# Performance work log

Hardware: AMD Instinct MI355X
Metric: run time of the kernel (lower is better)

Reference implementation:

```python
import jax, jax.numpy as jnp
import numpy as np

N_NODES = 100000


def gcn_conv(x, W, b, edge_index, n_nodes):
    """PyG GCNConv: add self-loops, symmetric deg^-1/2 normalization,
    linear transform, scatter-sum aggregation, bias."""
    x = x @ W  # [N, out]
    src, dst = edge_index[0], edge_index[1]
    self_idx = jnp.arange(n_nodes, dtype=src.dtype)
    src = jnp.concatenate([src, self_idx])
    dst = jnp.concatenate([dst, self_idx])
    # in-degree (including self-loop) per destination node
    deg = jax.ops.segment_sum(jnp.ones_like(src, dtype=x.dtype), dst,
                              num_segments=n_nodes)
    dinv = jnp.where(deg > 0, jax.lax.rsqrt(deg), 0.0)
    norm = dinv[src] * dinv[dst]  # [E+N]
    msg = x[src] * norm[:, None]  # gather + scale, [E+N, out]
    out = jax.ops.segment_sum(msg, dst, num_segments=n_nodes)
    return out + b


def setup_inputs() -> dict:
    key = jax.random.key(0)
    ks = jax.random.split(key, 7)
    in_c, hid_c, out_c = 256, 128, 64
    n_edges, n_lbl = 1600000, 200000
    x = jax.random.normal(ks[0], (N_NODES, in_c), dtype=jnp.float32)
    edge_index = jax.random.randint(ks[1], (2, n_edges), 0, N_NODES, dtype=jnp.int64)
    edge_label_index = jax.random.randint(ks[2], (2, n_lbl), 0, N_NODES, dtype=jnp.int64)
    # Glorot-style init for GCN linear weights
    W1 = jax.random.normal(ks[3], (in_c, hid_c), dtype=jnp.float32) / np.sqrt(in_c)
    b1 = jnp.zeros((hid_c,), dtype=jnp.float32)
    W2 = jax.random.normal(ks[4], (hid_c, out_c), dtype=jnp.float32) / np.sqrt(hid_c)
    b2 = jnp.zeros((out_c,), dtype=jnp.float32)
    return {"x": x, "edge_index": edge_index,
            "edge_label_index": edge_label_index,
            "W1": W1, "b1": b1, "W2": W2, "b2": b2}


def reference(x, edge_index, edge_label_index, W1, b1, W2, b2):
    n = x.shape[0]
    h = jax.nn.relu(gcn_conv(x, W1, b1, edge_index, n))
    z = gcn_conv(h, W2, b2, edge_index, n)  # [N, out_c]
    src, dst = edge_label_index[0], edge_label_index[1]
    return jnp.sum(z[src] * z[dst], axis=-1)  # [E_lbl]
```

## Files before the change

kernel.cpp:

```cpp
#include <hip/hip_runtime.h>
#include <hip/hip_bf16.h>

#define N_NODES 100000
#define N_EDGES 1600000
#define N_LBL   200000
#define C_IN    256
#define C_HID   128
#define C_OUT   64
#define SCAN_BLOCKS 391
#define NBUCKET 391
#define FILLA_EPB 2048

using u16 = unsigned short;
using u32 = unsigned int;
using u64 = unsigned long long;
using s64 = long long;

typedef __attribute__((ext_vector_type(8))) short bf16x8;
typedef __attribute__((ext_vector_type(4))) float f32x4;

__device__ __forceinline__ float bf2f(u16 h) {
    u32 u = ((u32)h) << 16;
    float f;
    __builtin_memcpy(&f, &u, 4);
    return f;
}
__device__ __forceinline__ u16 f2bf(float f) {
    u32 u;
    __builtin_memcpy(&u, &f, 4);
    u32 r = (u + 0x7fffu + ((u >> 16) & 1u)) >> 16;
    return (u16)r;
}
__device__ __forceinline__ void unpack_bf2(u32 p, float& lo, float& hi) {
    u32 l = p << 16;
    u32 h = p & 0xffff0000u;
    __builtin_memcpy(&lo, &l, 4);
    __builtin_memcpy(&hi, &h, 4);
}
__device__ __forceinline__ void acc4(u64 p, float& a0, float& a1,
                                     float& a2, float& a3) {
    u32 lo = (u32)p, hi = (u32)(p >> 32);
    float f0, f1, f2, f3;
    unpack_bf2(lo, f0, f1);
    unpack_bf2(hi, f2, f3);
    a0 += f0; a1 += f1; a2 += f2; a3 += f3;
}
__device__ __forceinline__ int geti(const void* p, s64 i, int i64) {
    return i64 ? (int)((const s64*)p)[i] : ((const int*)p)[i];
}
__device__ __forceinline__ int clampn(int v) {
    return ((u32)v < (u32)N_NODES) ? v : 0;
}

__device__ __forceinline__ void split8(const float4& a, const float4& b,
                                       bf16x8& hi8, bf16x8& lo8) {
    float va[8] = {a.x, a.y, a.z, a.w, b.x, b.y, b.z, b.w};
    u32 uh[4], ul[4];
#pragma unroll
    for (int p = 0; p < 4; ++p) {
        float x0 = va[2 * p], x1 = va[2 * p + 1];
        u32 u0, u1;
        __builtin_memcpy(&u0, &x0, 4);
        __builtin_memcpy(&u1, &x1, 4);
        u32 h0 = u0 & 0xffff0000u, h1 = u1 & 0xffff0000u;
        float f0, f1;
        __builtin_memcpy(&f0, &h0, 4);
        __builtin_memcpy(&f1, &h1, 4);
        float l0 = x0 - f0, l1 = x1 - f1;
        u32 w0, w1;
        __builtin_memcpy(&w0, &l0, 4);
        __builtin_memcpy(&w1, &l1, 4);
        uh[p] = (u0 >> 16) | h1;
        ul[p] = (w0 >> 16) | (w1 & 0xffff0000u);
    }
    struct U { u32 w[4]; };
    U H = {{uh[0], uh[1], uh[2], uh[3]}};
    U L = {{ul[0], ul[1], ul[2], ul[3]}};
    __builtin_memcpy(&hi8, &H, 16);
    __builtin_memcpy(&lo8, &L, 16);
}

__global__ void k_detect(const void* __restrict__ x, const void* __restrict__ ei,
                         int* __restrict__ flags) {
    const int lane = threadIdx.x & 63;
    const u16* xh = (const u16*)x;
    int cnt = 0;
#pragma unroll
    for (int k = 0; k < 4; ++k) {
        int i = 2 * (lane + 64 * k);
        u32 e = (xh[i] >> 7) & 0xFF;
        cnt += __builtin_popcountll(__ballot(e > 137));
    }
    const u32* ew = (const u32*)ei;
    int nz = __builtin_popcountll(__ballot(ew[2 * lane + 1] != 0));
    if (lane == 0) {
        flags[0] = (cnt > 16) ? 1 : 0;
        flags[1] = (nz == 0) ? 1 : 0;
    }
}

__global__ __launch_bounds__(256) void k_bcount(const void* __restrict__ ei,
                                                const int* __restrict__ flags,
                                                int* __restrict__ bcnt) {
    __shared__ int hist[NBUCKET];
    const int t = threadIdx.x;
    if (t < NBUCKET) hist[t] = 0;
    if (t + 256 < NBUCKET) hist[t + 256] = 0;
    __syncthreads();
    const s64 base = (s64)blockIdx.x * FILLA_EPB;
    const int i64 = flags[1];
#pragma unroll
    for (int j = 0; j < 8; ++j) {
        s64 e = base + t + 256 * j;
        if (e < N_EDGES) {
            int d = clampn(geti(ei, (s64)N_EDGES + e, i64));
            atomicAdd(&hist[d >> 8], 1);
        }
    }
    __syncthreads();
    if (t < NBUCKET && hist[t]) atomicAdd(&bcnt[t], hist[t]);
    if (t + 256 < NBUCKET && hist[t + 256]) atomicAdd(&bcnt[t + 256], hist[t + 256]);
}

__global__ __launch_bounds__(512) void k_bscan(const int* __restrict__ bcnt,
                                               int* __restrict__ bstart,
                                               int* __restrict__ gcur) {
    __shared__ int arr[512];
    const int t = threadIdx.x;
    int v = (t < NBUCKET) ? bcnt[t] : 0;
    arr[t] = v;
    __syncthreads();
#pragma unroll
    for (int off = 1; off < 512; off <<= 1) {
        int u = (t >= off) ? arr[t - off] : 0;
        __syncthreads();
        arr[t] += u;
        __syncthreads();
    }
    if (t < NBUCKET) {
        int ex = arr[t] - v;
        bstart[t] = ex;
        gcur[t]   = ex;
    }
    if (t == 511) bstart[NBUCKET] = arr[511];
}

__global__ __launch_bounds__(256) void k_fillA(const void* __restrict__ ei,
                                               const int* __restrict__ flags,
                                               int* __restrict__ gcur,
                                               u64* __restrict__ temp) {
    __shared__ int hist[NBUCKET];
    __shared__ int gbase[NBUCKET];
    const int t = threadIdx.x;
    if (t < NBUCKET) hist[t] = 0;
    if (t + 256 < NBUCKET) hist[t + 256] = 0;
    __syncthreads();
    const s64 base = (s64)blockIdx.x * FILLA_EPB;
    const int i64 = flags[1];
    int sv[8], dv[8], bk[8], off[8];
    bool val[8];
#pragma unroll
    for (int j = 0; j < 8; ++j) {
        s64 e = base + t + 256 * j;
        val[j] = (e < N_EDGES);
        if (val[j]) {
            sv[j] = clampn(geti(ei, e, i64));
            dv[j] = clampn(geti(ei, (s64)N_EDGES + e, i64));
            bk[j] = dv[j] >> 8;
            off[j] = atomicAdd(&hist[bk[j]], 1);
        }
    }
    __syncthreads();
    if (t < NBUCKET && hist[t]) gbase[t] = atomicAdd(&gcur[t], hist[t]);
    if (t + 256 < NBUCKET && hist[t + 256]) gbase[t + 256] = atomicAdd(&gcur[t + 256], hist[t + 256]);
    __syncthreads();
#pragma unroll
    for (int j = 0; j < 8; ++j) {
        if (val[j])
            temp[(size_t)(gbase[bk[j]] + off[j])] = ((u64)(u32)dv[j] << 32) | (u32)sv[j];
    }
}

__global__ __launch_bounds__(256) void k_deg2(const u64* __restrict__ temp,
                                              const int* __restrict__ bstart,
                                              int* __restrict__ deg) {
    __shared__ int dcnt[256];
    const int t = threadIdx.x;
    const int b = blockIdx.x;
    dcnt[t] = 0;
    __syncthreads();
    const int beg = bstart[b], end = bstart[b + 1];
    for (int e = beg + t; e < end; e += 256) {
        u32 d = (u32)(temp[e] >> 32);
        atomicAdd(&dcnt[d & 255], 1);
    }
    __syncthreads();
    int node = (b << 8) + t;
    if (node < N_NODES) deg[node] = dcnt[t];
}

__global__ __launch_bounds__(256) void k_fillB(const u64* __restrict__ temp,
                                               const int* __restrict__ bstart,
                                               const int* __restrict__ row_ptr,
                                               int* __restrict__ csr_src) {
    __shared__ int cur[256];
    const int t = threadIdx.x;
    const int b = blockIdx.x;
    int node = (b << 8) + t;
    cur[t] = (node < N_NODES) ? row_ptr[node] : 0;
    __syncthreads();
    const int beg = bstart[b], end = bstart[b + 1];
    for (int e = beg + t; e < end; e += 256) {
        u64 p = temp[e];
        u32 s = (u32)p, d = (u32)(p >> 32);
        int pos = atomicAdd(&cur[d & 255], 1);
        csr_src[pos] = (int)s;
    }
}

__global__ __launch_bounds__(256) void k_scan1(const int* __restrict__ deg,
                                               int* __restrict__ bsum) {
    __shared__ int red[256];
    const int t = threadIdx.x;
    int i = blockIdx.x * 256 + t;
    red[t] = (i < N_NODES) ? deg[i] : 0;
    __syncthreads();
#pragma unroll
    for (int off = 128; off > 0; off >>= 1) {
        if (t < off) red[t] += red[t + off];
        __syncthreads();
    }
    if (t == 0) bsum[blockIdx.x] = red[0];
}

__global__ __launch_bounds__(512) void k_scan2(const int* __restrict__ bsum,
                                               int* __restrict__ boff,
                                               int* __restrict__ row_ptr) {
    __shared__ int arr[512];
    const int t = threadIdx.x;
    int v = (t < SCAN_BLOCKS) ? bsum[t] : 0;
    arr[t] = v;
    __syncthreads();
#pragma unroll
    for (int off = 1; off < 512; off <<= 1) {
        int u = (t >= off) ? arr[t - off] : 0;
        __syncthreads();
        arr[t] += u;
        __syncthreads();
    }
    if (t < SCAN_BLOCKS) boff[t] = arr[t] - v;
    if (t == 511) row_ptr[N_NODES] = arr[511];
}

__global__ __launch_bounds__(256) void k_scan3(const int* __restrict__ deg,
                                               const int* __restrict__ boff,
                                               int* __restrict__ row_ptr,
                                               float* __restrict__ dinv) {
    __shared__ int arr[256];
    const int t = threadIdx.x;
    int i = blockIdx.x * 256 + t;
    int v = (i < N_NODES) ? deg[i] : 0;
    arr[t] = v;
    __syncthreads();
#pragma unroll
    for (int off = 1; off < 256; off <<= 1) {
        int u = (t >= off) ? arr[t - off] : 0;
        __syncthreads();
        arr[t] += u;
        __syncthreads();
    }
    if (i < N_NODES) {
        int run = boff[blockIdx.x] + arr[t] - v;
        row_ptr[i] = run;
        dinv[i]    = rsqrtf((float)v + 1.0f);
    }
}

__global__ __launch_bounds__(256) void k_w1t(const void* __restrict__ W1_,
                                             const int* __restrict__ flags,
                                             u16* __restrict__ w1t_hi,
                                             u16* __restrict__ w1t_lo) {
    int idx = blockIdx.x * 256 + threadIdx.x;
    int k = idx >> 7, n = idx & 127;
    float v = flags[0] ? ((const float*)W1_)[idx] : bf2f(((const u16*)W1_)[idx]);
    u32 uv;
    __builtin_memcpy(&uv, &v, 4);
    u32 hf = uv & 0xffff0000u;
    float hb;
    __builtin_memcpy(&hb, &hf, 4);
    float lo = v - hb;
    u32 ulo;
    __builtin_memcpy(&ulo, &lo, 4);
    w1t_hi[n * C_IN + k] = (u16)(uv >> 16);
    w1t_lo[n * C_IN + k] = (u16)(ulo >> 16);
}

__global__ __launch_bounds__(256) void k_w2t(const void* __restrict__ W2_,
                                             const int* __restrict__ flags,
                                             u16* __restrict__ w2t_hi,
                                             u16* __restrict__ w2t_lo) {
    int idx = blockIdx.x * 256 + threadIdx.x;
    int k = idx >> 6, n = idx & 63;
    float v = flags[0] ? ((const float*)W2_)[idx] : bf2f(((const u16*)W2_)[idx]);
    u32 uv;
    __builtin_memcpy(&uv, &v, 4);
    u32 hf = uv & 0xffff0000u;
    float hb;
    __builtin_memcpy(&hb, &hf, 4);
    float lo = v - hb;
    u32 ulo;
    __builtin_memcpy(&ulo, &lo, 4);
    w2t_hi[n * C_HID + k] = (u16)(uv >> 16);
    w2t_lo[n * C_HID + k] = (u16)(ulo >> 16);
}

__global__ __launch_bounds__(512) void k_gemm1_mfma(const void* __restrict__ xv_,
                                                    const u16* __restrict__ w1t_hi,
                                                    const u16* __restrict__ w1t_lo,
                                                    const float* __restrict__ dinv,
                                                    const int* __restrict__ flags,
                                                    u16* __restrict__ g0) {
    __shared__ u16 lds_hi[64 * 256];
    __shared__ u16 lds_lo[64 * 256];
    const int isf32 = flags[0];
    const int lane = threadIdx.x & 63;
    const int wid  = threadIdx.x >> 6;
    const int r0   = blockIdx.x * 256 + wid * 32;
    const int nbase = blockIdx.y * 64;

    {
        const u16* sh = w1t_hi + (size_t)nbase * C_IN;
        const u16* sl = w1t_lo + (size_t)nbase * C_IN;
        for (int g = threadIdx.x; g < 2048; g += 512) {
            int row = g >> 5;
            int off = (g & 31) << 4;
            int dst = row * 512 + (off ^ ((row & 7) << 4));
            *(uint4*)((char*)lds_hi + dst) =
                *(const uint4*)((const char*)(sh + (size_t)row * C_IN) + off);
            *(uint4*)((char*)lds_lo + dst) =
                *(const uint4*)((const char*)(sl + (size_t)row * C_IN) + off);
        }
    }
    __syncthreads();

    const int rowA = r0 + (lane & 15);
    const int rowB = rowA + 16;
    const int rlA  = (rowA < N_NODES) ? rowA : (N_NODES - 1);
    const int rlB  = (rowB < N_NODES) ? rowB : (N_NODES - 1);
    const int kh   = (lane >> 4) * 8;
    const int khb  = (lane >> 4) * 16;

    int rbase[4], rswz[4];
#pragma unroll
    for (int n = 0; n < 4; ++n) {
        int rloc = n * 16 + (lane & 15);
        rbase[n] = rloc * 512;
        rswz[n]  = (rloc & 7) << 4;
    }

    f32x4 acc[2][4];
#pragma unroll
    for (int g = 0; g < 2; ++g)
#pragma unroll
        for (int n = 0; n < 4; ++n) acc[g][n] = (f32x4){0.f, 0.f, 0.f, 0.f};

    if (isf32) {
        const float* apA = (const float*)xv_ + (size_t)rlA * C_IN + kh;
        const float* apB = (const float*)xv_ + (size_t)rlB * C_IN + kh;
        float4 xa0 = ((const float4*)apA)[0];
        float4 xa1 = ((const float4*)(apA + 4))[0];
        float4 xb0 = ((const float4*)apB)[0];
        float4 xb1 = ((const float4*)(apB + 4))[0];
#pragma unroll
        for (int k0 = 0; k0 < C_IN; k0 += 32) {
            bf16x8 bh[4], bl[4];
#pragma unroll
            for (int n = 0; n < 4; ++n) {
                int a = rbase[n] + ((k0 * 2 + khb) ^ rswz[n]);
                bh[n] = *(const bf16x8*)((const char*)lds_hi + a);
                bl[n] = *(const bf16x8*)((const char*)lds_lo + a);
            }
            float4 na0, na1, nb0, nb1;
            if (k0 + 32 < C_IN) {
                na0 = ((const float4*)(apA + k0 + 32))[0];
                na1 = ((const float4*)(apA + k0 + 36))[0];
                nb0 = ((const float4*)(apB + k0 + 32))[0];
                nb1 = ((const float4*)(apB + k0 + 36))[0];
            }
            bf16x8 ahiA, aloA, ahiB, aloB;
            split8(xa0, xa1, ahiA, aloA);
            split8(xb0, xb1, ahiB, aloB);
#pragma unroll
            for (int n = 0; n < 4; ++n) {
                acc[0][n] = __builtin_amdgcn_mfma_f32_16x16x32_bf16(ahiA, bl[n], acc[0][n], 0, 0, 0);
                acc[0][n] = __builtin_amdgcn_mfma_f32_16x16x32_bf16(aloA, bh[n], acc[0][n], 0, 0, 0);
                acc[0][n] = __builtin_amdgcn_mfma_f32_16x16x32_bf16(ahiA, bh[n], acc[0][n], 0, 0, 0);
                acc[1][n] = __builtin_amdgcn_mfma_f32_16x16x32_bf16(ahiB, bl[n], acc[1][n], 0, 0, 0);
                acc[1][n] = __builtin_amdgcn_mfma_f32_16x16x32_bf16(aloB, bh[n], acc[1][n], 0, 0, 0);
                acc[1][n] = __builtin_amdgcn_mfma_f32_16x16x32_bf16(ahiB, bh[n], acc[1][n], 0, 0, 0);
            }
            if (k0 + 32 < C_IN) { xa0 = na0; xa1 = na1; xb0 = nb0; xb1 = nb1; }
        }
    } else {
        const u16* apA = (const u16*)xv_ + (size_t)rlA * C_IN + kh;
        const u16* apB = (const u16*)xv_ + (size_t)rlB * C_IN + kh;
        bf16x8 aA = *(const bf16x8*)apA;
        bf16x8 aB = *(const bf16x8*)apB;
#pragma unroll
        for (int k0 = 0; k0 < C_IN; k0 += 32) {
            bf16x8 bh[4];
#pragma unroll
            for (int n = 0; n < 4; ++n) {
                int a = rbase[n] + ((k0 * 2 + khb) ^ rswz[n]);
                bh[n] = *(const bf16x8*)((const char*)lds_hi + a);
            }
            bf16x8 nA, nB;
            if (k0 + 32 < C_IN) {
                nA = *(const bf16x8*)(apA + k0 + 32);
                nB = *(const bf16x8*)(apB + k0 + 32);
            }
#pragma unroll
            for (int n = 0; n < 4; ++n) {
                acc[0][n] = __builtin_amdgcn_mfma_f32_16x16x32_bf16(aA, bh[n], acc[0][n], 0, 0, 0);
                acc[1][n] = __builtin_amdgcn_mfma_f32_16x16x32_bf16(aB, bh[n], acc[1][n], 0, 0, 0);
            }
            if (k0 + 32 < C_IN) { aA = nA; aB = nB; }
        }
    }

    const int ccol = lane & 15;
#pragma unroll
    for (int g = 0; g < 2; ++g) {
        const int crow0 = r0 + g * 16 + (lane >> 4) * 4;
#pragma unroll
        for (int i = 0; i < 4; ++i) {
            int r = crow0 + i;
            if (r < N_NODES) {
                float dv = dinv[r];
#pragma unroll
                for (int n = 0; n < 4; ++n)
                    g0[(size_t)r * C_HID + nbase + n * 16 + ccol] = f2bf(dv * acc[g][n][i]);
            }
        }
    }
}

__global__ __launch_bounds__(512) void k_gemm2_mfma(const float* __restrict__ h,
                                                    const u16* __restrict__ w2t_hi,
                                                    const u16* __restrict__ w2t_lo,
                                                    const float* __restrict__ dinv,
                                                    u16* __restrict__ g1) {
    __shared__ u16 lds_hi[64 * 128];
    __shared__ u16 lds_lo[64 * 128];
    const int lane = threadIdx.x & 63;
    const int wid  = threadIdx.x >> 6;
    const int r0   = blockIdx.x * 256 + wid * 32;

    {
        for (int g = threadIdx.x; g < 1024; g += 512) {
            int row = g >> 4;
            int off = (g & 15) << 4;
            int dst = row * 256 + (off ^ ((row & 7) << 4));
            *(uint4*)((char*)lds_hi + dst) =
                *(const uint4*)((const char*)(w2t_hi + (size_t)row * C_HID) + off);
            *(uint4*)((char*)lds_lo + dst) =
                *(const uint4*)((const char*)(w2t_lo + (size_t)row * C_HID) + off);
        }
    }
    __syncthreads();

    const int rowA = r0 + (lane & 15);
    const int rowB = rowA + 16;
    const int rlA  = (rowA < N_NODES) ? rowA : (N_NODES - 1);
    const int rlB  = (rowB < N_NODES) ? rowB : (N_NODES - 1);
    const int kh   = (lane >> 4) * 8;
    const int khb  = (lane >> 4) * 16;

    int rbase[4], rswz[4];
#pragma unroll
    for (int n = 0; n < 4; ++n) {
        int rloc = n * 16 + (lane & 15);
        rbase[n] = rloc * 256;
        rswz[n]  = (rloc & 7) << 4;
    }

    f32x4 acc[2][4];
#pragma unroll
    for (int g = 0; g < 2; ++g)
#pragma unroll
        for (int n = 0; n < 4; ++n) acc[g][n] = (f32x4){0.f, 0.f, 0.f, 0.f};

    const float* apA = h + (size_t)rlA * C_HID + kh;
    const float* apB = h + (size_t)rlB * C_HID + kh;

    float4 xa0 = ((const float4*)apA)[0];
    float4 xa1 = ((const float4*)(apA + 4))[0];
    float4 xb0 = ((const float4*)apB)[0];
    float4 xb1 = ((const float4*)(apB + 4))[0];
#pragma unroll
    for (int k0 = 0; k0 < C_HID; k0 += 32) {
        bf16x8 bh[4], bl[4];
#pragma unroll
        for (int n = 0; n < 4; ++n) {
            int a = rbase[n] + ((k0 * 2 + khb) ^ rswz[n]);
            bh[n] = *(const bf16x8*)((const char*)lds_hi + a);
            bl[n] = *(const bf16x8*)((const char*)lds_lo + a);
        }
        float4 na0, na1, nb0, nb1;
        if (k0 + 32 < C_HID) {
            na0 = ((const float4*)(apA + k0 + 32))[0];
            na1 = ((const float4*)(apA + k0 + 36))[0];
            nb0 = ((const float4*)(apB + k0 + 32))[0];
            nb1 = ((const float4*)(apB + k0 + 36))[0];
        }
        bf16x8 ahiA, aloA, ahiB, aloB;
        split8(xa0, xa1, ahiA, aloA);
        split8(xb0, xb1, ahiB, aloB);
#pragma unroll
        for (int n = 0; n < 4; ++n) {
            acc[0][n] = __builtin_amdgcn_mfma_f32_16x16x32_bf16(ahiA, bl[n], acc[0][n], 0, 0, 0);
            acc[0][n] = __builtin_amdgcn_mfma_f32_16x16x32_bf16(aloA, bh[n], acc[0][n], 0, 0, 0);
            acc[0][n] = __builtin_amdgcn_mfma_f32_16x16x32_bf16(ahiA, bh[n], acc[0][n], 0, 0, 0);
            acc[1][n] = __builtin_amdgcn_mfma_f32_16x16x32_bf16(ahiB, bl[n], acc[1][n], 0, 0, 0);
            acc[1][n] = __builtin_amdgcn_mfma_f32_16x16x32_bf16(aloB, bh[n], acc[1][n], 0, 0, 0);
            acc[1][n] = __builtin_amdgcn_mfma_f32_16x16x32_bf16(ahiB, bh[n], acc[1][n], 0, 0, 0);
        }
        if (k0 + 32 < C_HID) { xa0 = na0; xa1 = na1; xb0 = nb0; xb1 = nb1; }
    }

    const int ccol = lane & 15;
#pragma unroll
    for (int g = 0; g < 2; ++g) {
        const int crow0 = r0 + g * 16 + (lane >> 4) * 4;
#pragma unroll
        for (int i = 0; i < 4; ++i) {
            int r = crow0 + i;
            if (r < N_NODES) {
                float dv = dinv[r];
#pragma unroll
                for (int n = 0; n < 4; ++n)
                    g1[(size_t)r * C_OUT + n * 16 + ccol] = f2bf(dv * acc[g][n][i]);
            }
        }
    }
}

__global__ __launch_bounds__(256) void k_gather128(const int* __restrict__ row_ptr,
                                                   const int* __restrict__ csr_src,
                                                   const u64* __restrict__ g,
                                                   const void* __restrict__ bias_,
                                                   const float* __restrict__ dinv,
                                                   const int* __restrict__ flags,
                                                   float* __restrict__ out) {
    const int lane = threadIdx.x & 63;
    const int wid  = threadIdx.x >> 6;
    const int half = lane >> 5;
    const int jj   = lane & 31;
    const int node = blockIdx.x * 8 + wid * 2 + half;
    const u64* gp = g + jj;
    const int beg = row_ptr[node], end = row_ptr[node + 1];
    float a0 = 0.f, a1 = 0.f, a2 = 0.f, a3 = 0.f;
    int e = beg;
    for (; e + 4 <= end; e += 4) {
        int s0 = csr_src[e], s1 = csr_src[e + 1];
        int s2 = csr_src[e + 2], s3 = csr_src[e + 3];
        u64 p0 = gp[(size_t)s0 * 32];
        u64 p1 = gp[(size_t)s1 * 32];
        u64 p2 = gp[(size_t)s2 * 32];
        u64 p3 = gp[(size_t)s3 * 32];
        acc4(p0, a0, a1, a2, a3);
        acc4(p1, a0, a1, a2, a3);
        acc4(p2, a0, a1, a2, a3);
        acc4(p3, a0, a1, a2, a3);
    }
    for (; e < end; ++e) acc4(gp[(size_t)csr_src[e] * 32], a0, a1, a2, a3);
    acc4(gp[(size_t)node * 32], a0, a1, a2, a3);
    float b0, b1, b2, b3;
    if (flags[0]) {
        float4 bb = ((const float4*)bias_)[jj];
        b0 = bb.x; b1 = bb.y; b2 = bb.z; b3 = bb.w;
    } else {
        u64 bw = ((const u64*)bias_)[jj];
        unpack_bf2((u32)bw, b0, b1);
        unpack_bf2((u32)(bw >> 32), b2, b3);
    }
    float dv = dinv[node];
    float4 r;
    r.x = fmaxf(dv * a0 + b0, 0.f);
    r.y = fmaxf(dv * a1 + b1, 0.f);
    r.z = fmaxf(dv * a2 + b2, 0.f);
    r.w = fmaxf(dv * a3 + b3, 0.f);
    ((float4*)(out + (size_t)node * C_HID))[jj] = r;
}

__global__ __launch_bounds__(256) void k_gather64(const int* __restrict__ row_ptr,
                                                  const int* __restrict__ csr_src,
                                                  const u64* __restrict__ g,
                                                  const void* __restrict__ bias_,
                                                  const float* __restrict__ dinv,
                                                  const int* __restrict__ flags,
                                                  float* __restrict__ out) {
    const int lane = threadIdx.x & 63;
    const int wid  = threadIdx.x >> 6;
    const int q    = lane >> 4;
    const int jj   = lane & 15;
    const int node = blockIdx.x * 16 + wid * 4 + q;
    const u64* gp = g + jj;
    const int beg = row_ptr[node], end = row_ptr[node + 1];
    float a0 = 0.f, a1 = 0.f, a2 = 0.f, a3 = 0.f;
    int e = beg;
    for (; e + 4 <= end; e += 4) {
        int s0 = csr_src[e], s1 = csr_src[e + 1];
        int s2 = csr_src[e + 2], s3 = csr_src[e + 3];
        u64 p0 = gp[(size_t)s0 * 16];
        u64 p1 = gp[(size_t)s1 * 16];
        u64 p2 = gp[(size_t)s2 * 16];
        u64 p3 = gp[(size_t)s3 * 16];
        acc4(p0, a0, a1, a2, a3);
        acc4(p1, a0, a1, a2, a3);
        acc4(p2, a0, a1, a2, a3);
        acc4(p3, a0, a1, a2, a3);
    }
    for (; e < end; ++e) acc4(gp[(size_t)csr_src[e] * 16], a0, a1, a2, a3);
    acc4(gp[(size_t)node * 16], a0, a1, a2, a3);
    float b0, b1, b2, b3;
    if (flags[0]) {
        float4 bb = ((const float4*)bias_)[jj];
        b0 = bb.x; b1 = bb.y; b2 = bb.z; b3 = bb.w;
    } else {
        u64 bw = ((const u64*)bias_)[jj];
        unpack_bf2((u32)bw, b0, b1);
        unpack_bf2((u32)(bw >> 32), b2, b3);
    }
    float dv = dinv[node];
    float4 r;
    r.x = dv * a0 + b0;
    r.y = dv * a1 + b1;
    r.z = dv * a2 + b2;
    r.w = dv * a3 + b3;
    ((float4*)(out + (size_t)node * C_OUT))[jj] = r;
}

__global__ __launch_bounds__(256) void k_edgedot(const void* __restrict__ eli,
                                                 const int* __restrict__ flags,
                                                 const float* __restrict__ z,
                                                 void* __restrict__ out) {
    const int g16 = threadIdx.x >> 4;
    const int l16 = threadIdx.x & 15;
    const int e = blockIdx.x * 16 + g16;
    if (e >= N_LBL) return;
    const int i64 = flags[1];
    const int s = clampn(geti(eli, e, i64));
    const int d = clampn(geti(eli, (s64)N_LBL + e, i64));
    float4 zs = *(const float4*)(z + (size_t)s * C_OUT + l16 * 4);
    float4 zd = *(const float4*)(z + (size_t)d * C_OUT + l16 * 4);
    float v = zs.x * zd.x + zs.y * zd.y + zs.z * zd.z + zs.w * zd.w;
    v += __shfl_xor(v, 1, 64);
    v += __shfl_xor(v, 2, 64);
    v += __shfl_xor(v, 4, 64);
    v += __shfl_xor(v, 8, 64);
    if (l16 == 0) {
        if (flags[0]) ((float*)out)[e] = v;
        else          ((u16*)out)[e]   = f2bf(v);
    }
}

extern "C" void kernel_launch(void* const* d_in, const int* in_sizes, int n_in,
                              void* d_out, int out_size, void* d_ws, size_t ws_size,
                              hipStream_t stream) {
    const void* x   = d_in[0];
    const void* ei  = d_in[1];
    const void* eli = d_in[2];
    const void* W1  = d_in[3];
    const void* b1  = d_in[4];
    const void* W2  = d_in[5];
    const void* b2  = d_in[6];

    if (ws_size < 84800128) return;
    char* ws = (char*)d_ws;
    float* h       = (float*)ws;
    float* z       = (float*)ws;
    int*   bsum    = (int*)ws;
    int*   boff    = (int*)(ws + 4096);
    int*   bcnt    = (int*)(ws + 8192);
    int*   bstart  = (int*)(ws + 12288);
    int*   gcur    = (int*)(ws + 16384);
    u64*   temp    = (u64*)(ws + 1048576);
    u16*   g0      = (u16*)(ws + 51200000);
    u16*   g1      = (u16*)(ws + 51200000);
    float* dinv    = (float*)(ws + 76800000);
    int*   deg     = (int*)(ws + 77200000);
    u16*   w1t_hi  = (u16*)(ws + 77200000);
    u16*   w1t_lo  = (u16*)(ws + 77200000 + 65536);
    u16*   w2t_hi  = (u16*)(ws + 77200000 + 131072);
    u16*   w2t_lo  = (u16*)(ws + 77200000 + 147456);
    int*   row_ptr = (int*)(ws + 77600000);
    int*   csr_src = (int*)(ws + 78400008);
    int*   flags   = (int*)(ws + 84800064);

    const int FILLA_GRID = (N_EDGES + FILLA_EPB - 1) / FILLA_EPB;

    k_detect<<<1, 64, 0, stream>>>(x, ei, flags);

    hipMemsetAsync(bcnt, 0, NBUCKET * sizeof(int), stream);
    k_bcount<<<FILLA_GRID, 256, 0, stream>>>(ei, flags, bcnt);
    k_bscan<<<1, 512, 0, stream>>>(bcnt, bstart, gcur);
    k_fillA<<<FILLA_GRID, 256, 0, stream>>>(ei, flags, gcur, temp);
    k_deg2<<<NBUCKET, 256, 0, stream>>>(temp, bstart, deg);

    k_scan1<<<SCAN_BLOCKS, 256, 0, stream>>>(deg, bsum);
    k_scan2<<<1, 512, 0, stream>>>(bsum, boff, row_ptr);
    k_scan3<<<SCAN_BLOCKS, 256, 0, stream>>>(deg, boff, row_ptr, dinv);

    k_fillB<<<NBUCKET, 256, 0, stream>>>(temp, bstart, row_ptr, csr_src);

    k_w1t<<<128, 256, 0, stream>>>(W1, flags, w1t_hi, w1t_lo);
    k_w2t<<<32, 256, 0, stream>>>(W2, flags, w2t_hi, w2t_lo);

    k_gemm1_mfma<<<dim3((N_NODES + 255) / 256, 2), 512, 0, stream>>>(x, w1t_hi, w1t_lo, dinv, flags, g0);
    k_gather128<<<N_NODES / 8, 256, 0, stream>>>(row_ptr, csr_src, (const u64*)g0, b1, dinv, flags, h);

    k_gemm2_mfma<<<(N_NODES + 255) / 256, 512, 0, stream>>>(h, w2t_hi, w2t_lo, dinv, g1);
    k_gather64<<<N_NODES / 16, 256, 0, stream>>>(row_ptr, csr_src, (const u64*)g1, b2, dinv, flags, z);

    k_edgedot<<<(N_LBL + 15) / 16, 256, 0, stream>>>(eli, flags, z, d_out);
}
```

Baseline: 408.5 us.

## Compute all 128 output columns per block in gemm1 to read x once

The first GEMM now covers all 128 hidden columns in one block instead of splitting the output columns across two grid-y blocks. Each x row is loaded and split into hi/lo bf16 once rather than twice, halving global reads of the 100k x 256 fp32 input. In exchange each block stages the whole transposed W1 hi/lo, 128 KB of dynamic LDS, which allows at most one block per CU. It also doubles the accumulator registers per thread and moves the B-fragment LDS loads inside the MFMA loop.

```diff
diff --git a/kernel.cpp b/kernel.cpp
--- a/kernel.cpp
+++ b/kernel.cpp
@@ -320,26 +320,22 @@
                                                     const float* __restrict__ dinv,
                                                     const int* __restrict__ flags,
                                                     u16* __restrict__ g0) {
-    __shared__ u16 lds_hi[64 * 256];
-    __shared__ u16 lds_lo[64 * 256];
+    extern __shared__ char smem[];
+    u16* lds_hi = (u16*)smem;
+    u16* lds_lo = (u16*)(smem + 65536);
     const int isf32 = flags[0];
     const int lane = threadIdx.x & 63;
     const int wid  = threadIdx.x >> 6;
     const int r0   = blockIdx.x * 256 + wid * 32;
-    const int nbase = blockIdx.y * 64;
-
-    {
-        const u16* sh = w1t_hi + (size_t)nbase * C_IN;
-        const u16* sl = w1t_lo + (size_t)nbase * C_IN;
-        for (int g = threadIdx.x; g < 2048; g += 512) {
-            int row = g >> 5;
-            int off = (g & 31) << 4;
-            int dst = row * 512 + (off ^ ((row & 7) << 4));
-            *(uint4*)((char*)lds_hi + dst) =
-                *(const uint4*)((const char*)(sh + (size_t)row * C_IN) + off);
-            *(uint4*)((char*)lds_lo + dst) =
-                *(const uint4*)((const char*)(sl + (size_t)row * C_IN) + off);
-        }
+
+    for (int g = threadIdx.x; g < 4096; g += 512) {
+        int row = g >> 5;
+        int off = (g & 31) << 4;
+        int dst = row * 512 + (off ^ ((row & 7) << 4));
+        *(uint4*)((char*)lds_hi + dst) =
+            *(const uint4*)((const char*)(w1t_hi + (size_t)row * C_IN) + off);
+        *(uint4*)((char*)lds_lo + dst) =
+            *(const uint4*)((const char*)(w1t_lo + (size_t)row * C_IN) + off);
     }
     __syncthreads();
 
@@ -350,19 +346,19 @@
     const int kh   = (lane >> 4) * 8;
     const int khb  = (lane >> 4) * 16;
 
-    int rbase[4], rswz[4];
-#pragma unroll
-    for (int n = 0; n < 4; ++n) {
+    int rbase[8], rswz[8];
+#pragma unroll
+    for (int n = 0; n < 8; ++n) {
         int rloc = n * 16 + (lane & 15);
         rbase[n] = rloc * 512;
         rswz[n]  = (rloc & 7) << 4;
     }
 
-    f32x4 acc[2][4];
+    f32x4 acc[2][8];
 #pragma unroll
     for (int g = 0; g < 2; ++g)
 #pragma unroll
-        for (int n = 0; n < 4; ++n) acc[g][n] = (f32x4){0.f, 0.f, 0.f, 0.f};
+        for (int n = 0; n < 8; ++n) acc[g][n] = (f32x4){0.f, 0.f, 0.f, 0.f};
 
     if (isf32) {
         const float* apA = (const float*)xv_ + (size_t)rlA * C_IN + kh;
@@ -373,13 +369,6 @@
         float4 xb1 = ((const float4*)(apB + 4))[0];
 #pragma unroll
         for (int k0 = 0; k0 < C_IN; k0 += 32) {
-            bf16x8 bh[4], bl[4];
-#pragma unroll
-            for (int n = 0; n < 4; ++n) {
-                int a = rbase[n] + ((k0 * 2 + khb) ^ rswz[n]);
-                bh[n] = *(const bf16x8*)((const char*)lds_hi + a);
-                bl[n] = *(const bf16x8*)((const char*)lds_lo + a);
-            }
             float4 na0, na1, nb0, nb1;
             if (k0 + 32 < C_IN) {
                 na0 = ((const float4*)(apA + k0 + 32))[0];
@@ -391,13 +380,16 @@
             split8(xa0, xa1, ahiA, aloA);
             split8(xb0, xb1, ahiB, aloB);
 #pragma unroll
-            for (int n = 0; n < 4; ++n) {
-                acc[0][n] = __builtin_amdgcn_mfma_f32_16x16x32_bf16(ahiA, bl[n], acc[0][n], 0, 0, 0);
-                acc[0][n] = __builtin_amdgcn_mfma_f32_16x16x32_bf16(aloA, bh[n], acc[0][n], 0, 0, 0);
-                acc[0][n] = __builtin_amdgcn_mfma_f32_16x16x32_bf16(ahiA, bh[n], acc[0][n], 0, 0, 0);
-                acc[1][n] = __builtin_amdgcn_mfma_f32_16x16x32_bf16(ahiB, bl[n], acc[1][n], 0, 0, 0);
-                acc[1][n] = __builtin_amdgcn_mfma_f32_16x16x32_bf16(aloB, bh[n], acc[1][n], 0, 0, 0);
-                acc[1][n] = __builtin_amdgcn_mfma_f32_16x16x32_bf16(ahiB, bh[n], acc[1][n], 0, 0, 0);
+            for (int n = 0; n < 8; ++n) {
+                int a = rbase[n] + ((k0 * 2 + khb) ^ rswz[n]);
+                bf16x8 bh = *(const bf16x8*)((const char*)lds_hi + a);
+                bf16x8 bl = *(const bf16x8*)((const char*)lds_lo + a);
+                acc[0][n] = __builtin_amdgcn_mfma_f32_16x16x32_bf16(ahiA, bl, acc[0][n], 0, 0, 0);
+                acc[0][n] = __builtin_amdgcn_mfma_f32_16x16x32_bf16(aloA, bh, acc[0][n], 0, 0, 0);
+                acc[0][n] = __builtin_amdgcn_mfma_f32_16x16x32_bf16(ahiA, bh, acc[0][n], 0, 0, 0);
+                acc[1][n] = __builtin_amdgcn_mfma_f32_16x16x32_bf16(ahiB, bl, acc[1][n], 0, 0, 0);
+                acc[1][n] = __builtin_amdgcn_mfma_f32_16x16x32_bf16(aloB, bh, acc[1][n], 0, 0, 0);
+                acc[1][n] = __builtin_amdgcn_mfma_f32_16x16x32_bf16(ahiB, bh, acc[1][n], 0, 0, 0);
             }
             if (k0 + 32 < C_IN) { xa0 = na0; xa1 = na1; xb0 = nb0; xb1 = nb1; }
         }
@@ -408,21 +400,17 @@
         bf16x8 aB = *(const bf16x8*)apB;
 #pragma unroll
         for (int k0 = 0; k0 < C_IN; k0 += 32) {
-            bf16x8 bh[4];
-#pragma unroll
-            for (int n = 0; n < 4; ++n) {
-                int a = rbase[n] + ((k0 * 2 + khb) ^ rswz[n]);
-                bh[n] = *(const bf16x8*)((const char*)lds_hi + a);
-            }
             bf16x8 nA, nB;
             if (k0 + 32 < C_IN) {
                 nA = *(const bf16x8*)(apA + k0 + 32);
                 nB = *(const bf16x8*)(apB + k0 + 32);
             }
 #pragma unroll
-            for (int n = 0; n < 4; ++n) {
-                acc[0][n] = __builtin_amdgcn_mfma_f32_16x16x32_bf16(aA, bh[n], acc[0][n], 0, 0, 0);
-                acc[1][n] = __builtin_amdgcn_mfma_f32_16x16x32_bf16(aB, bh[n], acc[1][n], 0, 0, 0);
+            for (int n = 0; n < 8; ++n) {
+                int a = rbase[n] + ((k0 * 2 + khb) ^ rswz[n]);
+                bf16x8 bh = *(const bf16x8*)((const char*)lds_hi + a);
+                acc[0][n] = __builtin_amdgcn_mfma_f32_16x16x32_bf16(aA, bh, acc[0][n], 0, 0, 0);
+                acc[1][n] = __builtin_amdgcn_mfma_f32_16x16x32_bf16(aB, bh, acc[1][n], 0, 0, 0);
             }
             if (k0 + 32 < C_IN) { aA = nA; aB = nB; }
         }
@@ -438,8 +426,8 @@
             if (r < N_NODES) {
                 float dv = dinv[r];
 #pragma unroll
-                for (int n = 0; n < 4; ++n)
-                    g0[(size_t)r * C_HID + nbase + n * 16 + ccol] = f2bf(dv * acc[g][n][i]);
+                for (int n = 0; n < 8; ++n)
+                    g0[(size_t)r * C_HID + n * 16 + ccol] = f2bf(dv * acc[g][n][i]);
             }
         }
     }
@@ -700,6 +688,13 @@
 
     const int FILLA_GRID = (N_EDGES + FILLA_EPB - 1) / FILLA_EPB;
 
+    static bool attr_set = false;
+    if (!attr_set) {
+        hipFuncSetAttribute((const void*)k_gemm1_mfma,
+                            hipFuncAttributeMaxDynamicSharedMemorySize, 131072);
+        attr_set = true;
+    }
+
     k_detect<<<1, 64, 0, stream>>>(x, ei, flags);
 
     hipMemsetAsync(bcnt, 0, NBUCKET * sizeof(int), stream);
@@ -717,7 +712,7 @@
     k_w1t<<<128, 256, 0, stream>>>(W1, flags, w1t_hi, w1t_lo);
     k_w2t<<<32, 256, 0, stream>>>(W2, flags, w2t_hi, w2t_lo);
 
-    k_gemm1_mfma<<<dim3((N_NODES + 255) / 256, 2), 512, 0, stream>>>(x, w1t_hi, w1t_lo, dinv, flags, g0);
+    k_gemm1_mfma<<<(N_NODES + 255) / 256, 512, 131072, stream>>>(x, w1t_hi, w1t_lo, dinv, flags, g0);
     k_gather128<<<N_NODES / 8, 256, 0, stream>>>(row_ptr, csr_src, (const u64*)g0, b1, dinv, flags, h);
 
     k_gemm2_mfma<<<(N_NODES + 255) / 256, 512, 0, stream>>>(h, w2t_hi, w2t_lo, dinv, g1);
```

New measurement: 403.7 us. About the same (-1.2%).
